# Kernel optimization log

Measured on AMD Instinct MI355X. Metric: run time of the kernel, lower is better.

## Reference

```python
import jax, jax.numpy as jnp
import numpy as np

N_NODES = 100000
N_EDGES = 1600000
N_FEAT = 128
HIDDEN = 64
N_CLASSES = 40


def setup_inputs() -> dict:
    key = jax.random.key(0)
    ks = jax.random.split(key, 4)
    x = jax.random.normal(ks[0], (N_NODES, N_FEAT), dtype=jnp.float32)
    edge_index = jax.random.randint(ks[1], (2, N_EDGES), 0, N_NODES, dtype=jnp.int64)
    # Glorot-style init like PyG GCNConv
    W1 = jax.random.normal(ks[2], (N_FEAT, HIDDEN), dtype=jnp.float32) * (1.0 / np.sqrt(N_FEAT))
    b1 = jnp.zeros((HIDDEN,), dtype=jnp.float32)
    W2 = jax.random.normal(ks[3], (HIDDEN, N_CLASSES), dtype=jnp.float32) * (1.0 / np.sqrt(HIDDEN))
    b2 = jnp.zeros((N_CLASSES,), dtype=jnp.float32)
    return {"x": x, "edge_index": edge_index, "W1": W1, "b1": b1, "W2": W2, "b2": b2}


def _gcn_conv(x, src, dst, norm, W, b, n_nodes):
    # PyG GCNConv: transform first, then normalized scatter-add aggregation
    h = x @ W                                   # [N, out]
    msg = h[src] * norm[:, None]                # [E+N, out] gather
    out = jax.ops.segment_sum(msg, dst, num_segments=n_nodes)  # scatter-add
    return out + b


def _norm_and_loops(edge_index, n_nodes):
    # add self-loops, symmetric normalization deg^{-1/2} A_hat deg^{-1/2}
    loop = jnp.arange(n_nodes, dtype=edge_index.dtype)
    src = jnp.concatenate([edge_index[0], loop])
    dst = jnp.concatenate([edge_index[1], loop])
    deg = jax.ops.segment_sum(jnp.ones_like(dst, dtype=jnp.float32), dst, num_segments=n_nodes)
    dinv = jnp.where(deg > 0, jax.lax.rsqrt(jnp.maximum(deg, 1.0)), 0.0)
    norm = dinv[src] * dinv[dst]
    return src, dst, norm


def reference(x, edge_index, W1, b1, W2, b2):
    n_nodes = x.shape[0]
    src, dst, norm = _norm_and_loops(edge_index, n_nodes)
    h = _gcn_conv(x, src, dst, norm, W1, b1, n_nodes)
    h = jax.nn.relu(h)
    h = _gcn_conv(h, src, dst, norm, W2, b2, n_nodes)
    return jax.nn.log_softmax(h, axis=1)
```

## Files before the change

### kernel.cpp

```cpp
#include <hip/hip_runtime.h>
#include <hip/hip_bf16.h>
#include <string.h>

#define N_FEAT 128
#define HIDDEN 64
#define N_CLS  40
#define SCAN_B 256
#define FILL_BLOCKS 1024

typedef __bf16 bf16x8 __attribute__((ext_vector_type(8)));
typedef float  f32x4  __attribute__((ext_vector_type(4)));

union Frag { unsigned u[4]; bf16x8 v; };


static __device__ inline unsigned pack_bf16(float a, float b) {
    unsigned ba = __float_as_uint(a);
    unsigned bb = __float_as_uint(b);
    unsigned ra = (ba + 0x7fffu + ((ba >> 16) & 1u)) >> 16;
    unsigned rb = (bb + 0x7fffu + ((bb >> 16) & 1u)) >> 16;
    return (ra & 0xffffu) | (rb << 16);
}

static __device__ inline float2 unpack_bf16(unsigned v) {
    return make_float2(__uint_as_float(v << 16), __uint_as_float(v & 0xffff0000u));
}


__global__ void detect_layout_kernel(const int* __restrict__ ei, int* __restrict__ flag) {
    int lane = threadIdx.x;
    int v = ei[2 * lane + 1];
    unsigned long long b = __ballot(v != 0);
    if (lane == 0) flag[0] = (b == 0ull) ? 1 : 0;
}


__global__ __launch_bounds__(256) void count_kernel(const int* __restrict__ ei,
                                                    const int* __restrict__ flag,
                                                    unsigned* __restrict__ deg, int E, int N) {
    int r  = blockIdx.x & 7;
    int gb = blockIdx.x >> 3;
    int nb = gridDim.x >> 3;
    int rng = (N + 7) >> 3;
    int lo = r * rng;
    int hi = min(N, lo + rng);
    bool is64 = (flag[0] != 0);
    const int* dstp = is64 ? (ei + 2 * E) : (ei + E);
    int stride = is64 ? 2 : 1;
    for (int e = gb * 256 + threadIdx.x; e < E; e += nb * 256) {
        int d = dstp[(size_t)e * stride];
        if (d >= lo && d < hi) atomicAdd(&deg[d], 1u);
    }
}


__global__ void scan1_kernel(const unsigned* __restrict__ deg, unsigned* __restrict__ rowptr,
                             unsigned* __restrict__ blockSums, float* __restrict__ dinv, int N) {
    __shared__ unsigned tmp[SCAN_B];
    int i = blockIdx.x * SCAN_B + threadIdx.x;
    unsigned v = (i < N) ? deg[i] : 0u;
    if (i < N) dinv[i] = rsqrtf((float)(v + 1u));
    tmp[threadIdx.x] = v;
    __syncthreads();
#pragma unroll
    for (int off = 1; off < SCAN_B; off <<= 1) {
        unsigned t = (threadIdx.x >= off) ? tmp[threadIdx.x - off] : 0u;
        __syncthreads();
        tmp[threadIdx.x] += t;
        __syncthreads();
    }
    if (i < N) rowptr[i] = tmp[threadIdx.x] - v;
    if (threadIdx.x == SCAN_B - 1) blockSums[blockIdx.x] = tmp[threadIdx.x];
}

__global__ void scan2_kernel(unsigned* __restrict__ blockSums, int nb) {
    __shared__ unsigned tmp[512];
    unsigned v = (threadIdx.x < (unsigned)nb) ? blockSums[threadIdx.x] : 0u;
    tmp[threadIdx.x] = v;
    __syncthreads();
#pragma unroll
    for (int off = 1; off < 512; off <<= 1) {
        unsigned t = (threadIdx.x >= (unsigned)off) ? tmp[threadIdx.x - off] : 0u;
        __syncthreads();
        tmp[threadIdx.x] += t;
        __syncthreads();
    }
    if (threadIdx.x < (unsigned)nb) blockSums[threadIdx.x] = tmp[threadIdx.x] - v;
}

__global__ void scan3_kernel(unsigned* __restrict__ rowptr, const unsigned* __restrict__ blockSums,
                             unsigned* __restrict__ cursor, int N) {
    int i = blockIdx.x * SCAN_B + threadIdx.x;
    if (i < N) {
        unsigned v = rowptr[i] + blockSums[blockIdx.x];
        rowptr[i] = v;
        cursor[i] = v;
    }
}


__global__ __launch_bounds__(256) void csr_fill_kernel(const int* __restrict__ ei,
                                                       const int* __restrict__ flag,
                                                       unsigned* __restrict__ cursor,
                                                       int* __restrict__ csr_src, int E, int N) {
    int r  = blockIdx.x & 7;
    int gb = blockIdx.x >> 3;
    int nb = gridDim.x >> 3;
    int rng = (N + 7) >> 3;
    int lo = r * rng;
    int hi = min(N, lo + rng);
    bool is64 = (flag[0] != 0);
    const int* dstp = is64 ? (ei + 2 * E) : (ei + E);
    int stride = is64 ? 2 : 1;
    for (int e = gb * 256 + threadIdx.x; e < E; e += nb * 256) {
        int d = dstp[(size_t)e * stride];
        if (d >= lo && d < hi) {
            int s = ei[(size_t)e * stride];
            unsigned slot = atomicAdd(&cursor[d], 1u);
            csr_src[slot] = s;
        }
    }
}


__global__ __launch_bounds__(256) void gemm1_mfma_kernel(const float* __restrict__ x,
                                                         const float* __restrict__ W1,
                                                         unsigned* __restrict__ h1b, int N) {
    int lane = threadIdx.x & 63;
    int quad = lane >> 4;
    int col  = lane & 15;

    Frag B[4][4];
#pragma unroll
    for (int c = 0; c < 4; ++c)
#pragma unroll
        for (int ks = 0; ks < 4; ++ks) {
            int n = c * 16 + col;
#pragma unroll
            for (int jj = 0; jj < 4; ++jj) {
                int k = ks * 32 + quad * 8 + 2 * jj;
                B[c][ks].u[jj] = pack_bf16(W1[k * HIDDEN + n], W1[(k + 1) * HIDDEN + n]);
            }
        }

    int wave_id = blockIdx.x * 4 + (threadIdx.x >> 6);
    int nwaves  = gridDim.x * 4;
    int ntiles  = (N + 15) >> 4;

    for (int rt = wave_id; rt < ntiles; rt += nwaves) {
        int rowA = rt * 16 + col;
        Frag A[4];
#pragma unroll
        for (int ks = 0; ks < 4; ++ks) {
            float4 a0 = make_float4(0.f, 0.f, 0.f, 0.f), a1 = a0;
            if (rowA < N) {
                const float4* ap = (const float4*)(x + (size_t)rowA * N_FEAT + ks * 32 + quad * 8);
                a0 = ap[0];
                a1 = ap[1];
            }
            A[ks].u[0] = pack_bf16(a0.x, a0.y);
            A[ks].u[1] = pack_bf16(a0.z, a0.w);
            A[ks].u[2] = pack_bf16(a1.x, a1.y);
            A[ks].u[3] = pack_bf16(a1.z, a1.w);
        }
        f32x4 acc[4] = {{0.f, 0.f, 0.f, 0.f}, {0.f, 0.f, 0.f, 0.f},
                        {0.f, 0.f, 0.f, 0.f}, {0.f, 0.f, 0.f, 0.f}};
#pragma unroll
        for (int ks = 0; ks < 4; ++ks)
#pragma unroll
            for (int c = 0; c < 4; ++c)
                acc[c] = __builtin_amdgcn_mfma_f32_16x16x32_bf16(A[ks].v, B[c][ks].v, acc[c], 0, 0, 0);

        int rowD = rt * 16 + quad * 4;
#pragma unroll
        for (int c = 0; c < 4; ++c)
#pragma unroll
            for (int r = 0; r < 4; ++r) {
                float v = acc[c][r];
                float nxt = __shfl_down(v, 1);
                int row = rowD + r;
                if (((lane & 1) == 0) && row < N)
                    h1b[(size_t)row * 32 + ((c * 16 + col) >> 1)] = pack_bf16(v, nxt);
            }
    }
}


__global__ __launch_bounds__(256) void gemm2_mfma_kernel(const unsigned* __restrict__ actb,
                                                         const float* __restrict__ W2,
                                                         unsigned* __restrict__ h2b, int N) {
    int lane = threadIdx.x & 63;
    int quad = lane >> 4;
    int col  = lane & 15;

    Frag B[3][2];
#pragma unroll
    for (int c = 0; c < 3; ++c)
#pragma unroll
        for (int ks = 0; ks < 2; ++ks) {
            int n = c * 16 + col;
#pragma unroll
            for (int jj = 0; jj < 4; ++jj) {
                int k = ks * 32 + quad * 8 + 2 * jj;
                float w0 = (n < N_CLS) ? W2[k * N_CLS + n] : 0.f;
                float w1 = (n < N_CLS) ? W2[(k + 1) * N_CLS + n] : 0.f;
                B[c][ks].u[jj] = pack_bf16(w0, w1);
            }
        }

    int wave_id = blockIdx.x * 4 + (threadIdx.x >> 6);
    int nwaves  = gridDim.x * 4;
    int ntiles  = (N + 15) >> 4;

    for (int rt = wave_id; rt < ntiles; rt += nwaves) {
        int rowA = rt * 16 + col;
        Frag A[2];
#pragma unroll
        for (int ks = 0; ks < 2; ++ks) {
            uint4 u = make_uint4(0u, 0u, 0u, 0u);
            if (rowA < N)
                u = *(const uint4*)(actb + (size_t)rowA * 32 + ks * 16 + quad * 4);
            A[ks].u[0] = u.x; A[ks].u[1] = u.y; A[ks].u[2] = u.z; A[ks].u[3] = u.w;
        }
        f32x4 acc[3] = {{0.f, 0.f, 0.f, 0.f}, {0.f, 0.f, 0.f, 0.f}, {0.f, 0.f, 0.f, 0.f}};
#pragma unroll
        for (int ks = 0; ks < 2; ++ks)
#pragma unroll
            for (int c = 0; c < 3; ++c)
                acc[c] = __builtin_amdgcn_mfma_f32_16x16x32_bf16(A[ks].v, B[c][ks].v, acc[c], 0, 0, 0);

        int rowD = rt * 16 + quad * 4;
#pragma unroll
        for (int c = 0; c < 3; ++c)
#pragma unroll
            for (int r = 0; r < 4; ++r) {
                float v = acc[c][r];
                float nxt = __shfl_down(v, 1);
                int row = rowD + r;
                int pair = (c * 16 + col) >> 1;
                if (((lane & 1) == 0) && pair < 20 && row < N)
                    h2b[(size_t)row * 20 + pair] = pack_bf16(v, nxt);
            }
    }
}


__global__ __launch_bounds__(256) void agg1_kernel(const unsigned* __restrict__ h1b,
                                                   const int* __restrict__ csr_src,
                                                   const unsigned* __restrict__ rowptr,
                                                   const unsigned* __restrict__ deg,
                                                   const float* __restrict__ dinv,
                                                   const float* __restrict__ b1,
                                                   unsigned* __restrict__ actb, int N) {
    int wave = threadIdx.x >> 6, lane = threadIdx.x & 63;
    int sub = lane >> 5, j = lane & 31;
    int d = blockIdx.x * 4 + wave;
    if (d >= N) return;
    float dv = dinv[d];
    float acc0 = 0.f, acc1 = 0.f;
    if (sub == 0) {
        float2 v = unpack_bf16(h1b[(size_t)d * 32 + j]);
        acc0 = dv * v.x; acc1 = dv * v.y;
    }
    unsigned beg = rowptr[d];
    int len = (int)deg[d];
    int i = 0;
    for (; i + 8 <= len; i += 8) {
        int s0 = csr_src[beg + i + sub];
        int s1 = csr_src[beg + i + 2 + sub];
        int s2 = csr_src[beg + i + 4 + sub];
        int s3 = csr_src[beg + i + 6 + sub];
        float w0 = dinv[s0], w1 = dinv[s1], w2 = dinv[s2], w3 = dinv[s3];
        unsigned v0 = h1b[(size_t)s0 * 32 + j];
        unsigned v1 = h1b[(size_t)s1 * 32 + j];
        unsigned v2 = h1b[(size_t)s2 * 32 + j];
        unsigned v3 = h1b[(size_t)s3 * 32 + j];
        float2 a0 = unpack_bf16(v0), a1 = unpack_bf16(v1);
        float2 a2 = unpack_bf16(v2), a3 = unpack_bf16(v3);
        acc0 += w0 * a0.x + w1 * a1.x + w2 * a2.x + w3 * a3.x;
        acc1 += w0 * a0.y + w1 * a1.y + w2 * a2.y + w3 * a3.y;
    }
    for (; i + 4 <= len; i += 4) {
        int sA = csr_src[beg + i + sub];
        int sB = csr_src[beg + i + 2 + sub];
        float wA = dinv[sA], wB = dinv[sB];
        float2 a = unpack_bf16(h1b[(size_t)sA * 32 + j]);
        float2 b = unpack_bf16(h1b[(size_t)sB * 32 + j]);
        acc0 += wA * a.x + wB * b.x;
        acc1 += wA * a.y + wB * b.y;
    }
    for (; i < len; i += 2) {
        int e = i + sub;
        if (e < len) {
            int s = csr_src[beg + e];
            float w = dinv[s];
            float2 a = unpack_bf16(h1b[(size_t)s * 32 + j]);
            acc0 += w * a.x;
            acc1 += w * a.y;
        }
    }
    acc0 += __shfl_xor(acc0, 32);
    acc1 += __shfl_xor(acc1, 32);
    if (sub == 0) {
        float2 bb = ((const float2*)b1)[j];
        float r0 = fmaxf(acc0 * dv + bb.x, 0.f);
        float r1 = fmaxf(acc1 * dv + bb.y, 0.f);
        actb[(size_t)d * 32 + j] = pack_bf16(r0, r1);
    }
}


__global__ __launch_bounds__(256) void agg2_lsm_kernel(const unsigned* __restrict__ h2b,
                                                       const int* __restrict__ csr_src,
                                                       const unsigned* __restrict__ rowptr,
                                                       const unsigned* __restrict__ deg,
                                                       const float* __restrict__ dinv,
                                                       const float* __restrict__ b2,
                                                       float* __restrict__ out, int N) {
    int wave = threadIdx.x >> 6, lane = threadIdx.x & 63;
    int sub = lane >> 5, j = lane & 31;
    bool act = (j < 20);
    int d = blockIdx.x * 4 + wave;
    if (d >= N) return;
    float dv = dinv[d];
    float acc0 = 0.f, acc1 = 0.f;
    if (sub == 0 && act) {
        float2 v = unpack_bf16(h2b[(size_t)d * 20 + j]);
        acc0 = dv * v.x; acc1 = dv * v.y;
    }
    unsigned beg = rowptr[d];
    int len = (int)deg[d];
    int i = 0;
    for (; i + 8 <= len; i += 8) {
        int s0 = csr_src[beg + i + sub];
        int s1 = csr_src[beg + i + 2 + sub];
        int s2 = csr_src[beg + i + 4 + sub];
        int s3 = csr_src[beg + i + 6 + sub];
        float w0 = dinv[s0], w1 = dinv[s1], w2 = dinv[s2], w3 = dinv[s3];
        if (act) {
            float2 a0 = unpack_bf16(h2b[(size_t)s0 * 20 + j]);
            float2 a1 = unpack_bf16(h2b[(size_t)s1 * 20 + j]);
            float2 a2 = unpack_bf16(h2b[(size_t)s2 * 20 + j]);
            float2 a3 = unpack_bf16(h2b[(size_t)s3 * 20 + j]);
            acc0 += w0 * a0.x + w1 * a1.x + w2 * a2.x + w3 * a3.x;
            acc1 += w0 * a0.y + w1 * a1.y + w2 * a2.y + w3 * a3.y;
        }
    }
    for (; i + 4 <= len; i += 4) {
        int sA = csr_src[beg + i + sub];
        int sB = csr_src[beg + i + 2 + sub];
        float wA = dinv[sA], wB = dinv[sB];
        if (act) {
            float2 a = unpack_bf16(h2b[(size_t)sA * 20 + j]);
            float2 b = unpack_bf16(h2b[(size_t)sB * 20 + j]);
            acc0 += wA * a.x + wB * b.x;
            acc1 += wA * a.y + wB * b.y;
        }
    }
    for (; i < len; i += 2) {
        int e = i + sub;
        if (e < len && act) {
            int s = csr_src[beg + e];
            float w = dinv[s];
            float2 a = unpack_bf16(h2b[(size_t)s * 20 + j]);
            acc0 += w * a.x;
            acc1 += w * a.y;
        }
    }
    acc0 += __shfl_xor(acc0, 32);
    acc1 += __shfl_xor(acc1, 32);
    float v0 = -1e30f, v1 = -1e30f;
    if (act) {
        float2 bb = ((const float2*)b2)[j];
        v0 = acc0 * dv + bb.x;
        v1 = acc1 * dv + bb.y;
    }
    float m = fmaxf(v0, v1);
#pragma unroll
    for (int off = 32; off > 0; off >>= 1)
        m = fmaxf(m, __shfl_xor(m, off));
    float ex = (act && sub == 0) ? (expf(v0 - m) + expf(v1 - m)) : 0.f;
#pragma unroll
    for (int off = 32; off > 0; off >>= 1)
        ex += __shfl_xor(ex, off);
    float ls = logf(ex);
    if (act && sub == 0) {
        float2* orow = (float2*)(out + (size_t)d * N_CLS);
        orow[j] = make_float2(v0 - m - ls, v1 - m - ls);
    }
}


static inline size_t align_up(size_t x) { return (x + 255) & ~(size_t)255; }

extern "C" void kernel_launch(void* const* d_in, const int* in_sizes, int n_in,
                              void* d_out, int out_size, void* d_ws, size_t ws_size,
                              hipStream_t stream) {
    const float* x  = (const float*)d_in[0];
    const int*   ei = (const int*)d_in[1];
    const float* W1 = (const float*)d_in[2];
    const float* b1 = (const float*)d_in[3];
    const float* W2 = (const float*)d_in[4];
    const float* b2 = (const float*)d_in[5];

    int N = in_sizes[0] / N_FEAT;
    int E = in_sizes[1] / 2;
    int nb = (N + SCAN_B - 1) / SCAN_B;

    char* ws = (char*)d_ws;
    int*      flag    = (int*)ws;       ws += 256;
    unsigned* deg     = (unsigned*)ws;  ws += align_up((size_t)N * 4);
    float*    dinv    = (float*)ws;     ws += align_up((size_t)N * 4);
    unsigned* rowptr  = (unsigned*)ws;  ws += align_up((size_t)N * 4);
    unsigned* cursor  = (unsigned*)ws;  ws += align_up((size_t)N * 4);
    unsigned* bsums   = (unsigned*)ws;  ws += align_up((size_t)nb * 4);
    int*      csr_src = (int*)ws;       ws += align_up((size_t)E * 4);
    unsigned* h1b     = (unsigned*)ws;  ws += align_up((size_t)N * 32 * 4);
    unsigned* actb    = (unsigned*)ws;  ws += align_up((size_t)N * 32 * 4);
    unsigned* h2b     = (unsigned*)ws;  ws += align_up((size_t)N * 20 * 4);

    hipMemsetAsync(deg, 0, (size_t)N * 4, stream);

    detect_layout_kernel<<<1, 64, 0, stream>>>(ei, flag);
    count_kernel<<<FILL_BLOCKS, 256, 0, stream>>>(ei, flag, deg, E, N);

    scan1_kernel<<<nb, SCAN_B, 0, stream>>>(deg, rowptr, bsums, dinv, N);
    scan2_kernel<<<1, 512, 0, stream>>>(bsums, nb);
    scan3_kernel<<<nb, SCAN_B, 0, stream>>>(rowptr, bsums, cursor, N);
    csr_fill_kernel<<<FILL_BLOCKS, 256, 0, stream>>>(ei, flag, cursor, csr_src, E, N);

    gemm1_mfma_kernel<<<512, 256, 0, stream>>>(x, W1, h1b, N);
    agg1_kernel<<<(N + 3) / 4, 256, 0, stream>>>(h1b, csr_src, rowptr, deg, dinv, b1, actb, N);

    gemm2_mfma_kernel<<<512, 256, 0, stream>>>(actb, W2, h2b, N);
    agg2_lsm_kernel<<<(N + 3) / 4, 256, 0, stream>>>(h2b, csr_src, rowptr, deg, dinv, b2, (float*)d_out, N);
}
```

Before: 377.6 us.

## Partition degree count and CSR fill by hardware XCC with dynamic chunking

The count and CSR-fill kernels now read the XCC id from a hardware register and assign each XCC a destination node range, so each node's atomics stay within one die's L2. Edge chunks are handed out dynamically through a per-XCC counter instead of a static block stride. Atomics are downgraded to workgroup scope so they avoid device-wide coherence traffic. This risks correctness if workgroup-scope atomics on global memory are not coherent across CUs within an XCC, and depends on the blocks actually covering every XCC.

```diff
diff --git a/kernel.cpp b/kernel.cpp
--- a/kernel.cpp
+++ b/kernel.cpp
@@ -7,11 +7,16 @@
 #define N_CLS  40
 #define SCAN_B 256
 #define FILL_BLOCKS 1024
+#define CHUNK_EDGES 2048
 
 typedef __bf16 bf16x8 __attribute__((ext_vector_type(8)));
 typedef float  f32x4  __attribute__((ext_vector_type(4)));
 
 union Frag { unsigned u[4]; bf16x8 v; };
+
+static __device__ inline int get_xcc() {
+    return (int)(__builtin_amdgcn_s_getreg((3 << 11) | 20) & 7u);
+}
 
 
 static __device__ inline unsigned pack_bf16(float a, float b) {
@@ -37,19 +42,31 @@
 
 __global__ __launch_bounds__(256) void count_kernel(const int* __restrict__ ei,
                                                     const int* __restrict__ flag,
-                                                    unsigned* __restrict__ deg, int E, int N) {
-    int r  = blockIdx.x & 7;
-    int gb = blockIdx.x >> 3;
-    int nb = gridDim.x >> 3;
-    int rng = (N + 7) >> 3;
+                                                    unsigned* __restrict__ deg,
+                                                    unsigned* __restrict__ ctr, int E, int N) {
+    int r = get_xcc();
+    int rng = (((N + 7) >> 3) + 15) & ~15;
     int lo = r * rng;
     int hi = min(N, lo + rng);
     bool is64 = (flag[0] != 0);
     const int* dstp = is64 ? (ei + 2 * E) : (ei + E);
     int stride = is64 ? 2 : 1;
-    for (int e = gb * 256 + threadIdx.x; e < E; e += nb * 256) {
-        int d = dstp[(size_t)e * stride];
-        if (d >= lo && d < hi) atomicAdd(&deg[d], 1u);
+    __shared__ unsigned chunk_s;
+    for (;;) {
+        if (threadIdx.x == 0)
+            chunk_s = __hip_atomic_fetch_add(&ctr[r * 64], 1u, __ATOMIC_RELAXED,
+                                             __HIP_MEMORY_SCOPE_WORKGROUP);
+        __syncthreads();
+        long long base = (long long)chunk_s * CHUNK_EDGES;
+        __syncthreads();
+        if (base >= E) break;
+        int end = (int)min((long long)E, base + CHUNK_EDGES);
+        for (int e = (int)base + threadIdx.x; e < end; e += 256) {
+            int d = dstp[(size_t)e * stride];
+            if (d >= lo && d < hi)
+                __hip_atomic_fetch_add(&deg[d], 1u, __ATOMIC_RELAXED,
+                                       __HIP_MEMORY_SCOPE_WORKGROUP);
+        }
     }
 }
 
@@ -102,22 +119,33 @@
 __global__ __launch_bounds__(256) void csr_fill_kernel(const int* __restrict__ ei,
                                                        const int* __restrict__ flag,
                                                        unsigned* __restrict__ cursor,
+                                                       unsigned* __restrict__ ctr,
                                                        int* __restrict__ csr_src, int E, int N) {
-    int r  = blockIdx.x & 7;
-    int gb = blockIdx.x >> 3;
-    int nb = gridDim.x >> 3;
-    int rng = (N + 7) >> 3;
+    int r = get_xcc();
+    int rng = (((N + 7) >> 3) + 15) & ~15;
     int lo = r * rng;
     int hi = min(N, lo + rng);
     bool is64 = (flag[0] != 0);
     const int* dstp = is64 ? (ei + 2 * E) : (ei + E);
     int stride = is64 ? 2 : 1;
-    for (int e = gb * 256 + threadIdx.x; e < E; e += nb * 256) {
-        int d = dstp[(size_t)e * stride];
-        if (d >= lo && d < hi) {
-            int s = ei[(size_t)e * stride];
-            unsigned slot = atomicAdd(&cursor[d], 1u);
-            csr_src[slot] = s;
+    __shared__ unsigned chunk_s;
+    for (;;) {
+        if (threadIdx.x == 0)
+            chunk_s = __hip_atomic_fetch_add(&ctr[r * 64], 1u, __ATOMIC_RELAXED,
+                                             __HIP_MEMORY_SCOPE_WORKGROUP);
+        __syncthreads();
+        long long base = (long long)chunk_s * CHUNK_EDGES;
+        __syncthreads();
+        if (base >= E) break;
+        int end = (int)min((long long)E, base + CHUNK_EDGES);
+        for (int e = (int)base + threadIdx.x; e < end; e += 256) {
+            int d = dstp[(size_t)e * stride];
+            if (d >= lo && d < hi) {
+                int s = ei[(size_t)e * stride];
+                unsigned slot = __hip_atomic_fetch_add(&cursor[d], 1u, __ATOMIC_RELAXED,
+                                                       __HIP_MEMORY_SCOPE_WORKGROUP);
+                csr_src[slot] = s;
+            }
         }
     }
 }
@@ -409,6 +437,7 @@
 
     char* ws = (char*)d_ws;
     int*      flag    = (int*)ws;       ws += 256;
+    unsigned* ctrs    = (unsigned*)ws;  ws += 4096;
     unsigned* deg     = (unsigned*)ws;  ws += align_up((size_t)N * 4);
     float*    dinv    = (float*)ws;     ws += align_up((size_t)N * 4);
     unsigned* rowptr  = (unsigned*)ws;  ws += align_up((size_t)N * 4);
@@ -419,15 +448,16 @@
     unsigned* actb    = (unsigned*)ws;  ws += align_up((size_t)N * 32 * 4);
     unsigned* h2b     = (unsigned*)ws;  ws += align_up((size_t)N * 20 * 4);
 
+    hipMemsetAsync(ctrs, 0, 4096, stream);
     hipMemsetAsync(deg, 0, (size_t)N * 4, stream);
 
     detect_layout_kernel<<<1, 64, 0, stream>>>(ei, flag);
-    count_kernel<<<FILL_BLOCKS, 256, 0, stream>>>(ei, flag, deg, E, N);
+    count_kernel<<<FILL_BLOCKS, 256, 0, stream>>>(ei, flag, deg, ctrs, E, N);
 
     scan1_kernel<<<nb, SCAN_B, 0, stream>>>(deg, rowptr, bsums, dinv, N);
     scan2_kernel<<<1, 512, 0, stream>>>(bsums, nb);
     scan3_kernel<<<nb, SCAN_B, 0, stream>>>(rowptr, bsums, cursor, N);
-    csr_fill_kernel<<<FILL_BLOCKS, 256, 0, stream>>>(ei, flag, cursor, csr_src, E, N);
+    csr_fill_kernel<<<FILL_BLOCKS, 256, 0, stream>>>(ei, flag, cursor, ctrs + 512, csr_src, E, N);
 
     gemm1_mfma_kernel<<<512, 256, 0, stream>>>(x, W1, h1b, N);
     agg1_kernel<<<(N + 3) / 4, 256, 0, stream>>>(h1b, csr_src, rowptr, deg, dinv, b1, actb, N);
```

Result: slower. 385.7 us (+2.1%).
